# Kernel optimization log

Measured on AMD Instinct MI355X. Metric: run time of the kernel, lower is better.

## Reference

```python
import jax, jax.numpy as jnp
import numpy as np

B, S, D = 4, 2048, 1024
H = 16
HD = D // H  # 64


def setup_inputs() -> dict:
    key = jax.random.key(0)
    ks = jax.random.split(key, 5)
    s = 0.02
    return {
        "x": jax.random.normal(ks[0], (B, S, D), dtype=jnp.float32),
        "w_qkv": jax.random.normal(ks[1], (D, 3 * D), dtype=jnp.float32) * s,
        "b_qkv": jnp.zeros((3 * D,), dtype=jnp.float32),
        "w_out": jax.random.normal(ks[2], (D, D), dtype=jnp.float32) * s,
        "b_out": jnp.zeros((D,), dtype=jnp.float32),
    }


def reference(x, w_qkv, b_qkv, w_out, b_out):
    b, s, d = x.shape
    qkv = x @ w_qkv + b_qkv                              # [b,s,3d]
    qkv = qkv.reshape(b, s, 3, H, HD)
    q = qkv[:, :, 0].transpose(0, 2, 1, 3)               # [b,h,s,hd]
    k = qkv[:, :, 1].transpose(0, 2, 1, 3)
    v = qkv[:, :, 2].transpose(0, 2, 1, 3)
    scale = 1.0 / jnp.sqrt(jnp.asarray(HD, dtype=x.dtype))
    scores = jnp.einsum("bhqd,bhkd->bhqk", q, k) * scale  # [b,h,s,s]
    causal = jnp.tril(jnp.ones((s, s), dtype=bool))
    scores = jnp.where(causal[None, None], scores, jnp.asarray(-jnp.inf, dtype=x.dtype))
    probs = jax.nn.softmax(scores, axis=-1)
    out = jnp.einsum("bhqk,bhkd->bhqd", probs, v)        # [b,h,s,hd]
    out = out.transpose(0, 2, 1, 3).reshape(b, s, d)
    return out @ w_out + b_out
```

## Files before the change

### kernel.cpp

```cpp
#include <hip/hip_runtime.h>
#include <hip/hip_bf16.h>

typedef __bf16 bf16_t;
typedef __bf16 bf16x4 __attribute__((ext_vector_type(4)));
typedef __bf16 bf16x8 __attribute__((ext_vector_type(8)));
typedef float f32x4 __attribute__((ext_vector_type(4)));

#define Bb 4
#define Ss 2048
#define Dd 1024
#define Hh 16
#define HDd 64

#define QSC 0.1803368801111244f

__device__ __forceinline__ void gld16(const bf16_t* g, bf16_t* l) {
  __builtin_amdgcn_global_load_lds(
      (const __attribute__((address_space(1))) unsigned int*)g,
      (__attribute__((address_space(3))) unsigned int*)l, 16, 0, 0);
}

__global__ __launch_bounds__(256) void prep(
    const float* __restrict__ x, bf16_t* __restrict__ Xc,
    const float* __restrict__ w_qkv, bf16_t* __restrict__ Wt1) {
  __shared__ bf16_t tile[32][33];
  const int b = blockIdx.x;
  const int tid = threadIdx.x;
  if (b < 8192) {
    int i = (b * 256 + tid) * 4;
    float4 v = *(const float4*)&x[i];
    bf16x4 o = {(bf16_t)v.x, (bf16_t)v.y, (bf16_t)v.z, (bf16_t)v.w};
    *(bf16x4*)&Xc[i] = o;
  } else {
    const int id = b - 8192;
    const int c0 = (id % 96) * 32, r0 = (id / 96) * 32;
    const int tx = tid & 31, ty = tid >> 5;
#pragma unroll
    for (int j = 0; j < 32; j += 8)
      tile[ty + j][tx] = (bf16_t)w_qkv[(size_t)(r0 + ty + j) * 3072 + c0 + tx];
    __syncthreads();
#pragma unroll
    for (int j = 0; j < 32; j += 8)
      Wt1[(size_t)(c0 + ty + j) * 1024 + r0 + tx] = tile[tx][ty + j];
  }
}

__global__ __launch_bounds__(256) void transpose_conv(
    const float* __restrict__ in, bf16_t* __restrict__ out, int R, int C) {
  __shared__ bf16_t tile[32][33];
  int c0 = blockIdx.x * 32, r0 = blockIdx.y * 32;
  int tx = threadIdx.x, ty = threadIdx.y;
#pragma unroll
  for (int j = 0; j < 32; j += 8)
    tile[ty + j][tx] = (bf16_t)in[(size_t)(r0 + ty + j) * C + c0 + tx];
  __syncthreads();
#pragma unroll
  for (int j = 0; j < 32; j += 8)
    out[(size_t)(c0 + ty + j) * R + r0 + tx] = tile[tx][ty + j];
}

template <int MODE>
__global__ __launch_bounds__(512, 2) void gemm_8p(
    const bf16_t* __restrict__ A, const bf16_t* __restrict__ Bt,
    const float* __restrict__ bias, float* __restrict__ outf,
    bf16_t* __restrict__ out0, bf16_t* __restrict__ out1,
    bf16_t* __restrict__ out2, int M, int N, int K) {
  const int tid = threadIdx.x;
  const int lane = tid & 63;
  const int wave = tid >> 6;
  const int quad = lane >> 4;
  const int lr = lane & 15;
  const int wr = wave >> 1;
  const int wc = wave & 1;
  const int m0 = blockIdx.y * 256;
  const int n0 = blockIdx.x * 128;

  __shared__ __align__(16) bf16_t As[3][256 * 64];
  __shared__ __align__(16) bf16_t Bs[3][128 * 64];

  const f32x4 zero = {0.f, 0.f, 0.f, 0.f};
  f32x4 acc[4][4];
#pragma unroll
  for (int mi = 0; mi < 4; ++mi)
#pragma unroll
    for (int ni = 0; ni < 4; ++ni) acc[mi][ni] = zero;

  int ar[4], ac[4], br[2], bc[2];
#pragma unroll
  for (int i = 0; i < 4; ++i) {
    int c = tid + i * 512;
    ar[i] = c >> 3;
    ac[i] = ((c & 7) ^ (ar[i] & 7)) * 8;
  }
#pragma unroll
  for (int i = 0; i < 2; ++i) {
    int c = tid + i * 512;
    br[i] = c >> 3;
    bc[i] = ((c & 7) ^ (br[i] & 7)) * 8;
  }

  const int nk = K >> 6;

  auto stageA = [&](int t, int s) {
    const int ko = t << 6;
#pragma unroll
    for (int i = 0; i < 4; ++i)
      gld16(&A[(size_t)(m0 + ar[i]) * K + ko + ac[i]],
            &As[s][(tid + i * 512) * 8]);
  };
  auto stageB = [&](int t, int s) {
    const int ko = t << 6;
#pragma unroll
    for (int i = 0; i < 2; ++i)
      gld16(&Bt[(size_t)(n0 + br[i]) * K + ko + bc[i]],
            &Bs[s][(tid + i * 512) * 8]);
  };

  stageA(0, 0); stageB(0, 0);
  stageA(1, 1); stageB(1, 1);
  asm volatile("s_waitcnt vmcnt(6)" ::: "memory");
  __builtin_amdgcn_s_barrier();

  const int sx = lr & 7;
  const int arow = wr * 64 + lr;
  const int brow = wc * 64 + lr;

  int scur = 0;
  for (int t = 0; t < nk; ++t) {
    const bf16_t* as = As[scur];
    const bf16_t* bs = Bs[scur];
    int s2 = scur + 2;
    if (s2 >= 3) s2 -= 3;
    const bool pre = (t + 2 < nk);
#pragma unroll
    for (int ks = 0; ks < 2; ++ks) {
      bf16x8 af[4], bfr[4];
      const int cx = (((ks << 2) | quad) ^ sx) * 8;
#pragma unroll
      for (int mi = 0; mi < 4; ++mi)
        af[mi] = *(const bf16x8*)&as[(arow + mi * 16) * 64 + cx];
#pragma unroll
      for (int ni = 0; ni < 4; ++ni)
        bfr[ni] = *(const bf16x8*)&bs[(brow + ni * 16) * 64 + cx];
      if (ks == 0) {
        if (pre) stageA(t + 2, s2);
      } else {
        if (pre) stageB(t + 2, s2);
      }
      __builtin_amdgcn_s_barrier();
      asm volatile("s_waitcnt lgkmcnt(0)" ::: "memory");
      __builtin_amdgcn_sched_barrier(0);
      __builtin_amdgcn_s_setprio(1);
#pragma unroll
      for (int mi = 0; mi < 4; ++mi)
#pragma unroll
        for (int ni = 0; ni < 4; ++ni)
          acc[mi][ni] = __builtin_amdgcn_mfma_f32_16x16x32_bf16(
              af[mi], bfr[ni], acc[mi][ni], 0, 0, 0);
      __builtin_amdgcn_s_setprio(0);
      if (ks == 0) {
        __builtin_amdgcn_s_barrier();
      } else if (t + 1 < nk) {
        if (pre)
          asm volatile("s_waitcnt vmcnt(6)" ::: "memory");
        else
          asm volatile("s_waitcnt vmcnt(0)" ::: "memory");
        __builtin_amdgcn_s_barrier();
      }
    }
    scur = (scur == 2) ? 0 : scur + 1;
  }

#pragma unroll
  for (int mi = 0; mi < 4; ++mi) {
    const int mbase = m0 + wr * 64 + mi * 16 + quad * 4;
#pragma unroll
    for (int ni = 0; ni < 4; ++ni) {
      const int n = n0 + wc * 64 + ni * 16 + lr;
      const float bv = bias[n];
      if (MODE == 1) {
#pragma unroll
        for (int r = 0; r < 4; ++r)
          outf[(size_t)(mbase + r) * N + n] = acc[mi][ni][r] + bv;
      } else {
        const int which = n >> 10;
        const int h = (n >> 6) & 15;
        const int hd = n & 63;
        const int b = mbase >> 11;
        const int s = mbase & 2047;
        if (which == 2) {
          bf16x4 pk = {(bf16_t)(acc[mi][ni][0] + bv),
                       (bf16_t)(acc[mi][ni][1] + bv),
                       (bf16_t)(acc[mi][ni][2] + bv),
                       (bf16_t)(acc[mi][ni][3] + bv)};
          *(bf16x4*)&out2[(((size_t)(b * Hh + h)) * HDd + hd) * Ss + s] = pk;
        } else {
          bf16_t* dst = (which == 0) ? out0 : out1;
          const float sc2 = (which == 0) ? QSC : 1.0f;
#pragma unroll
          for (int r = 0; r < 4; ++r)
            dst[(((size_t)(b * Hh + h)) * Ss + s + r) * HDd + hd] =
                (bf16_t)((acc[mi][ni][r] + bv) * sc2);
        }
      }
    }
  }
}

__global__ __launch_bounds__(256) void attn_kernel(
    const bf16_t* __restrict__ Qg, const bf16_t* __restrict__ Kg,
    const bf16_t* __restrict__ Vtg, bf16_t* __restrict__ Og) {
  const int tid = threadIdx.x;
  const int lane = tid & 63;
  const int wave = tid >> 6;
  const int quad = lane >> 4;
  const int lr = lane & 15;
  const int l7 = lr & 7;

  const int bid = blockIdx.x;
  const int xcd = bid & 7;
  const int j = bid >> 3;
  const int bh = xcd * 8 + (j >> 3);
  const int p = j & 7;
  const int b = bh >> 4;
  const int h = bh & 15;
  const int wq = wave * 32;

  const bf16_t* Qp = Qg + (size_t)bh * Ss * HDd;
  const bf16_t* Kp = Kg + (size_t)bh * Ss * HDd;
  const bf16_t* Vp = Vtg + (size_t)bh * HDd * Ss;

  __shared__ bf16_t Ks[2][64 * 64];
  __shared__ bf16_t Vts[2][64 * 64];
  __shared__ bf16_t Ps[4][32 * 64];

  bf16x8 kreg[2], vreg[2];
  const int r0 = tid >> 3;
  const int c0 = (tid & 7) * 8;
  const int swz = ((tid & 7) ^ ((tid >> 3) & 7)) * 8;

  const f32x4 zero = {0.f, 0.f, 0.f, 0.f};

#pragma unroll
  for (int i = 0; i < 2; ++i) {
    kreg[i] = *(const bf16x8*)&Kp[(size_t)(r0 + i * 32) * HDd + c0];
    vreg[i] = *(const bf16x8*)&Vp[(size_t)(r0 + i * 32) * Ss + c0];
  }

  int cur = 0;
  for (int half = 0; half < 2; ++half) {
    const int qt = half ? p : 15 - p;
    const int qbase = qt * 128;
    const int ktiles = qt * 2 + 2;

    bf16x8 bq[2][2];
#pragma unroll
    for (int qt2 = 0; qt2 < 2; ++qt2)
#pragma unroll
      for (int kk2 = 0; kk2 < 2; ++kk2)
        bq[qt2][kk2] = *(const bf16x8*)&Qp[(size_t)(qbase + wq + qt2 * 16 +
                                                    lr) *
                                               HDd +
                                           kk2 * 32 + quad * 8];

    f32x4 oacc[4][2];
#pragma unroll
    for (int dt = 0; dt < 4; ++dt)
#pragma unroll
      for (int qt2 = 0; qt2 < 2; ++qt2) oacc[dt][qt2] = zero;
    float l_run[2] = {0.f, 0.f};

    for (int kt = 0; kt < ktiles; ++kt) {
      const int kbase = kt * 64;

#pragma unroll
      for (int i = 0; i < 2; ++i) {
        *(bf16x8*)&Ks[cur][(r0 + i * 32) * 64 + swz] = kreg[i];
        *(bf16x8*)&Vts[cur][(r0 + i * 32) * 64 + swz] = vreg[i];
      }
      __syncthreads();

      const int nkb = (kt + 1 < ktiles) ? kbase + 64 : 0;
#pragma unroll
      for (int i = 0; i < 2; ++i) {
        kreg[i] = *(const bf16x8*)&Kp[(size_t)(nkb + r0 + i * 32) * HDd + c0];
        vreg[i] = *(const bf16x8*)&Vp[(size_t)(r0 + i * 32) * Ss + nkb + c0];
      }

      f32x4 sacc[4][2];
#pragma unroll
      for (int kt4 = 0; kt4 < 4; ++kt4)
#pragma unroll
        for (int qt2 = 0; qt2 < 2; ++qt2) sacc[kt4][qt2] = zero;
#pragma unroll
      for (int kk2 = 0; kk2 < 2; ++kk2) {
        const int rsl = (((kk2 << 2) | quad) ^ l7) * 8;
        bf16x8 ak[4];
#pragma unroll
        for (int kt4 = 0; kt4 < 4; ++kt4)
          ak[kt4] = *(const bf16x8*)&Ks[cur][(kt4 * 16 + lr) * 64 + rsl];
#pragma unroll
        for (int kt4 = 0; kt4 < 4; ++kt4)
#pragma unroll
          for (int qt2 = 0; qt2 < 2; ++qt2)
            sacc[kt4][qt2] = __builtin_amdgcn_mfma_f32_16x16x32_bf16(
                ak[kt4], bq[qt2][kk2], sacc[kt4][qt2], 0, 0, 0);
      }

      const bool edge = (kt >= 2 * qt);
#pragma unroll
      for (int kk2 = 0; kk2 < 2; ++kk2) {
#pragma unroll
        for (int k4 = 0; k4 < 2; ++k4) {
          const int kt4 = kk2 * 2 + k4;
          const int psl = ((kt4 * 2 + (quad >> 1)) ^ l7) * 8 + (quad & 1) * 4;
#pragma unroll
          for (int qt2 = 0; qt2 < 2; ++qt2) {
#pragma unroll
            for (int r = 0; r < 4; ++r) {
              float s = sacc[kt4][qt2][r];
              if (edge) {
                const int qg = qbase + wq + qt2 * 16 + lr;
                const int kg = kbase + kt4 * 16 + quad * 4 + r;
                if (kg > qg) s = -1e30f;
              }
              const float pv = __builtin_amdgcn_exp2f(s);
              sacc[kt4][qt2][r] = pv;
              l_run[qt2] += pv;
            }
            bf16x4 pk = {(bf16_t)sacc[kt4][qt2][0], (bf16_t)sacc[kt4][qt2][1],
                         (bf16_t)sacc[kt4][qt2][2],
                         (bf16_t)sacc[kt4][qt2][3]};
            *(bf16x4*)&Ps[wave][(qt2 * 16 + lr) * 64 + psl] = pk;
          }
        }
        const int rsl = (((kk2 << 2) | quad) ^ l7) * 8;
        bf16x8 av[4], bp[2];
#pragma unroll
        for (int dt = 0; dt < 4; ++dt)
          av[dt] = *(const bf16x8*)&Vts[cur][(dt * 16 + lr) * 64 + rsl];
#pragma unroll
        for (int qt2 = 0; qt2 < 2; ++qt2)
          bp[qt2] = *(const bf16x8*)&Ps[wave][(qt2 * 16 + lr) * 64 + rsl];
#pragma unroll
        for (int dt = 0; dt < 4; ++dt)
#pragma unroll
          for (int qt2 = 0; qt2 < 2; ++qt2)
            oacc[dt][qt2] = __builtin_amdgcn_mfma_f32_16x16x32_bf16(
                av[dt], bp[qt2], oacc[dt][qt2], 0, 0, 0);
      }
      cur ^= 1;
    }

#pragma unroll
    for (int qt2 = 0; qt2 < 2; ++qt2) {
      l_run[qt2] += __shfl_xor(l_run[qt2], 16, 64);
      l_run[qt2] += __shfl_xor(l_run[qt2], 32, 64);
    }

#pragma unroll
    for (int qt2 = 0; qt2 < 2; ++qt2) {
      const float inv = 1.f / l_run[qt2];
      const int qg = qbase + wq + qt2 * 16 + lr;
#pragma unroll
      for (int dt = 0; dt < 4; ++dt) {
        bf16x4 ov = {(bf16_t)(oacc[dt][qt2][0] * inv),
                     (bf16_t)(oacc[dt][qt2][1] * inv),
                     (bf16_t)(oacc[dt][qt2][2] * inv),
                     (bf16_t)(oacc[dt][qt2][3] * inv)};
        *(bf16x4*)&Og[((size_t)b * Ss + qg) * Dd + h * HDd + dt * 16 +
                      quad * 4] = ov;
      }
    }
  }
}

extern "C" void kernel_launch(void* const* d_in, const int* in_sizes, int n_in,
                              void* d_out, int out_size, void* d_ws,
                              size_t ws_size, hipStream_t stream) {
  const float* x = (const float*)d_in[0];
  const float* w_qkv = (const float*)d_in[1];
  const float* b_qkv = (const float*)d_in[2];
  const float* w_out = (const float*)d_in[3];
  const float* b_out = (const float*)d_in[4];
  float* out = (float*)d_out;

  bf16_t* Kb = (bf16_t*)d_ws;
  bf16_t* Vt = Kb + (size_t)Bb * Hh * Ss * HDd;
  bf16_t* slot3 = Vt + (size_t)Bb * Hh * Ss * HDd;
  bf16_t* Wt1 = slot3;
  bf16_t* Ob = slot3;
  bf16_t* Wt2 = Kb;
  bf16_t* Qb = (bf16_t*)d_out;
  bf16_t* Xc = (bf16_t*)d_out + (size_t)8192 * 1024;

  prep<<<11264, 256, 0, stream>>>(x, Xc, w_qkv, Wt1);

  gemm_8p<0><<<dim3(24, 32), 512, 0, stream>>>(
      Xc, Wt1, b_qkv, nullptr, Qb, Kb, Vt, 8192, 3072, 1024);

  attn_kernel<<<dim3(512), 256, 0, stream>>>(Qb, Kb, Vt, Ob);

  transpose_conv<<<dim3(32, 32), dim3(32, 8), 0, stream>>>(w_out, Wt2, 1024,
                                                           1024);

  gemm_8p<1><<<dim3(8, 32), 512, 0, stream>>>(
      Ob, Wt2, b_out, out, nullptr, nullptr, nullptr, 8192, 1024, 1024);
}
```

Before: 252.5 us.

## Load K/V fragments directly from global into registers, dropping shared staging

Removes the shared-memory double-buffered K/V tiles and the per-tile __syncthreads. Each wave now loads its MFMA operand fragments for K and V^T straight from global/L2 into registers, with K prefetched one tile ahead via register ping-pong in a 2x unrolled loop. It also sets launch_bounds occupancy to 2. Block-level sync and LDS traffic go away, but each of the four waves now refetches the same K/V data, multiplying global/L2 load traffic.

Result: slower. 318.6 us (+26.2%).

```diff
diff --git a/kernel.cpp b/kernel.cpp
--- a/kernel.cpp
+++ b/kernel.cpp
@@ -207,7 +207,7 @@
   }
 }
 
-__global__ __launch_bounds__(256) void attn_kernel(
+__global__ __launch_bounds__(256, 2) void attn_kernel(
     const bf16_t* __restrict__ Qg, const bf16_t* __restrict__ Kg,
     const bf16_t* __restrict__ Vtg, bf16_t* __restrict__ Og) {
   const int tid = threadIdx.x;
@@ -230,24 +230,13 @@
   const bf16_t* Kp = Kg + (size_t)bh * Ss * HDd;
   const bf16_t* Vp = Vtg + (size_t)bh * HDd * Ss;
 
-  __shared__ bf16_t Ks[2][64 * 64];
-  __shared__ bf16_t Vts[2][64 * 64];
   __shared__ bf16_t Ps[4][32 * 64];
 
-  bf16x8 kreg[2], vreg[2];
-  const int r0 = tid >> 3;
-  const int c0 = (tid & 7) * 8;
-  const int swz = ((tid & 7) ^ ((tid >> 3) & 7)) * 8;
-
   const f32x4 zero = {0.f, 0.f, 0.f, 0.f};
 
-#pragma unroll
-  for (int i = 0; i < 2; ++i) {
-    kreg[i] = *(const bf16x8*)&Kp[(size_t)(r0 + i * 32) * HDd + c0];
-    vreg[i] = *(const bf16x8*)&Vp[(size_t)(r0 + i * 32) * Ss + c0];
-  }
-
-  int cur = 0;
+  const int kfo = lr * HDd + quad * 8;
+  const size_t vfo = (size_t)lr * Ss + quad * 8;
+
   for (int half = 0; half < 2; ++half) {
     const int qt = half ? p : 15 - p;
     const int qbase = qt * 128;
@@ -270,87 +259,79 @@
       for (int qt2 = 0; qt2 < 2; ++qt2) oacc[dt][qt2] = zero;
     float l_run[2] = {0.f, 0.f};
 
-    for (int kt = 0; kt < ktiles; ++kt) {
-      const int kbase = kt * 64;
-
-#pragma unroll
-      for (int i = 0; i < 2; ++i) {
-        *(bf16x8*)&Ks[cur][(r0 + i * 32) * 64 + swz] = kreg[i];
-        *(bf16x8*)&Vts[cur][(r0 + i * 32) * 64 + swz] = vreg[i];
-      }
-      __syncthreads();
-
-      const int nkb = (kt + 1 < ktiles) ? kbase + 64 : 0;
-#pragma unroll
-      for (int i = 0; i < 2; ++i) {
-        kreg[i] = *(const bf16x8*)&Kp[(size_t)(nkb + r0 + i * 32) * HDd + c0];
-        vreg[i] = *(const bf16x8*)&Vp[(size_t)(r0 + i * 32) * Ss + nkb + c0];
-      }
-
-      f32x4 sacc[4][2];
-#pragma unroll
-      for (int kt4 = 0; kt4 < 4; ++kt4)
-#pragma unroll
-        for (int qt2 = 0; qt2 < 2; ++qt2) sacc[kt4][qt2] = zero;
-#pragma unroll
-      for (int kk2 = 0; kk2 < 2; ++kk2) {
-        const int rsl = (((kk2 << 2) | quad) ^ l7) * 8;
-        bf16x8 ak[4];
-#pragma unroll
-        for (int kt4 = 0; kt4 < 4; ++kt4)
-          ak[kt4] = *(const bf16x8*)&Ks[cur][(kt4 * 16 + lr) * 64 + rsl];
-#pragma unroll
-        for (int kt4 = 0; kt4 < 4; ++kt4)
-#pragma unroll
-          for (int qt2 = 0; qt2 < 2; ++qt2)
-            sacc[kt4][qt2] = __builtin_amdgcn_mfma_f32_16x16x32_bf16(
-                ak[kt4], bq[qt2][kk2], sacc[kt4][qt2], 0, 0, 0);
-      }
-
-      const bool edge = (kt >= 2 * qt);
-#pragma unroll
-      for (int kk2 = 0; kk2 < 2; ++kk2) {
-#pragma unroll
-        for (int k4 = 0; k4 < 2; ++k4) {
-          const int kt4 = kk2 * 2 + k4;
-          const int psl = ((kt4 * 2 + (quad >> 1)) ^ l7) * 8 + (quad & 1) * 4;
-#pragma unroll
-          for (int qt2 = 0; qt2 < 2; ++qt2) {
-#pragma unroll
-            for (int r = 0; r < 4; ++r) {
-              float s = sacc[kt4][qt2][r];
-              if (edge) {
-                const int qg = qbase + wq + qt2 * 16 + lr;
-                const int kg = kbase + kt4 * 16 + quad * 4 + r;
-                if (kg > qg) s = -1e30f;
-              }
-              const float pv = __builtin_amdgcn_exp2f(s);
-              sacc[kt4][qt2][r] = pv;
-              l_run[qt2] += pv;
-            }
-            bf16x4 pk = {(bf16_t)sacc[kt4][qt2][0], (bf16_t)sacc[kt4][qt2][1],
-                         (bf16_t)sacc[kt4][qt2][2],
-                         (bf16_t)sacc[kt4][qt2][3]};
-            *(bf16x4*)&Ps[wave][(qt2 * 16 + lr) * 64 + psl] = pk;
-          }
-        }
-        const int rsl = (((kk2 << 2) | quad) ^ l7) * 8;
-        bf16x8 av[4], bp[2];
-#pragma unroll
-        for (int dt = 0; dt < 4; ++dt)
-          av[dt] = *(const bf16x8*)&Vts[cur][(dt * 16 + lr) * 64 + rsl];
-#pragma unroll
-        for (int qt2 = 0; qt2 < 2; ++qt2)
-          bp[qt2] = *(const bf16x8*)&Ps[wave][(qt2 * 16 + lr) * 64 + rsl];
-#pragma unroll
-        for (int dt = 0; dt < 4; ++dt)
-#pragma unroll
-          for (int qt2 = 0; qt2 < 2; ++qt2)
-            oacc[dt][qt2] = __builtin_amdgcn_mfma_f32_16x16x32_bf16(
-                av[dt], bp[qt2], oacc[dt][qt2], 0, 0, 0);
-      }
-      cur ^= 1;
-    }
+    bf16x8 ka[4][2], kb_[4][2];
+#pragma unroll
+    for (int kt4 = 0; kt4 < 4; ++kt4)
+#pragma unroll
+      for (int kk2 = 0; kk2 < 2; ++kk2)
+        ka[kt4][kk2] =
+            *(const bf16x8*)&Kp[(size_t)(kt4 * 16) * HDd + kk2 * 32 + kfo];
+
+#define ATTN_BODY(KT, KC, KN)                                                 \
+  {                                                                           \
+    const int kbase = (KT)*64;                                                \
+    const int nkb = ((KT) + 1 < ktiles) ? kbase + 64 : 0;                     \
+                                            \
+    _Pragma("unroll") for (int kt4 = 0; kt4 < 4; ++kt4)                       \
+        _Pragma("unroll") for (int kk2 = 0; kk2 < 2; ++kk2)                   \
+        KN[kt4][kk2] = *(const bf16x8*)&Kp[(size_t)(nkb + kt4 * 16) * HDd +   \
+                                           kk2 * 32 + kfo];                   \
+              \
+    bf16x8 vf[4][2];                                                          \
+    _Pragma("unroll") for (int dt = 0; dt < 4; ++dt)                          \
+        _Pragma("unroll") for (int kk2 = 0; kk2 < 2; ++kk2)                   \
+        vf[dt][kk2] =                                                         \
+            *(const bf16x8*)&Vp[(size_t)(dt * 16) * Ss + kbase + kk2 * 32 +   \
+                                vfo];                                         \
+                                                           \
+    f32x4 sacc[4][2];                                                         \
+    _Pragma("unroll") for (int kt4 = 0; kt4 < 4; ++kt4)                       \
+        _Pragma("unroll") for (int qt2 = 0; qt2 < 2; ++qt2) sacc[kt4][qt2] =  \
+        zero;                                                                 \
+    _Pragma("unroll") for (int kk2 = 0; kk2 < 2; ++kk2)                       \
+        _Pragma("unroll") for (int kt4 = 0; kt4 < 4; ++kt4)                   \
+        _Pragma("unroll") for (int qt2 = 0; qt2 < 2; ++qt2) sacc[kt4][qt2] =  \
+        __builtin_amdgcn_mfma_f32_16x16x32_bf16(KC[kt4][kk2], bq[qt2][kk2],   \
+                                                sacc[kt4][qt2], 0, 0, 0);     \
+    const bool edge = ((KT) >= 2 * qt);                                       \
+     \
+    _Pragma("unroll") for (int kk2 = 0; kk2 < 2; ++kk2) {                     \
+      _Pragma("unroll") for (int k4 = 0; k4 < 2; ++k4) {                      \
+        const int kt4 = kk2 * 2 + k4;                                         \
+        const int psl = ((kt4 * 2 + (quad >> 1)) ^ l7) * 8 + (quad & 1) * 4;  \
+        _Pragma("unroll") for (int qt2 = 0; qt2 < 2; ++qt2) {                 \
+          _Pragma("unroll") for (int r = 0; r < 4; ++r) {                     \
+            float s = sacc[kt4][qt2][r];                                      \
+            if (edge) {                                                       \
+              const int qg = qbase + wq + qt2 * 16 + lr;                      \
+              const int kg = kbase + kt4 * 16 + quad * 4 + r;                 \
+              if (kg > qg) s = -1e30f;                                        \
+            }                                                                 \
+            const float pv = __builtin_amdgcn_exp2f(s);                       \
+            sacc[kt4][qt2][r] = pv;                                           \
+            l_run[qt2] += pv;                                                 \
+          }                                                                   \
+          bf16x4 pk = {(bf16_t)sacc[kt4][qt2][0], (bf16_t)sacc[kt4][qt2][1],  \
+                       (bf16_t)sacc[kt4][qt2][2], (bf16_t)sacc[kt4][qt2][3]}; \
+          *(bf16x4*)&Ps[wave][(qt2 * 16 + lr) * 64 + psl] = pk;               \
+        }                                                                     \
+      }                                                                       \
+      const int rsl = (((kk2 << 2) | quad) ^ l7) * 8;                         \
+      bf16x8 bp[2];                                                           \
+      _Pragma("unroll") for (int qt2 = 0; qt2 < 2; ++qt2) bp[qt2] =           \
+          *(const bf16x8*)&Ps[wave][(qt2 * 16 + lr) * 64 + rsl];              \
+      _Pragma("unroll") for (int dt = 0; dt < 4; ++dt)                        \
+          _Pragma("unroll") for (int qt2 = 0; qt2 < 2; ++qt2) oacc[dt][qt2] = \
+          __builtin_amdgcn_mfma_f32_16x16x32_bf16(vf[dt][kk2], bp[qt2],       \
+                                                  oacc[dt][qt2], 0, 0, 0);    \
+    }                                                                         \
+  }
+
+    for (int kt = 0; kt < ktiles; kt += 2) {
+      ATTN_BODY(kt, ka, kb_);
+      ATTN_BODY(kt + 1, kb_, ka);
+    }
+#undef ATTN_BODY
 
 #pragma unroll
     for (int qt2 = 0; qt2 < 2; ++qt2) {
```
